# Kernel optimization log

Hardware: AMD Instinct MI355X
Metric: run time of the kernel (lower is better)

## Reference

```python
import jax, jax.numpy as jnp
import numpy as np

B, T, C, HEADS = 4, 2305, 384, 6
BN_EPS = 1e-5


def setup_inputs() -> dict:
    key = jax.random.key(0)
    ks = jax.random.split(key, 24)
    d = {
        'x': jax.random.normal(ks[0], (B, T, C), dtype=jnp.float32),
        'h': 48,
        'w': 48,
        # depthwise conv kernels (groups=C, no bias): OIHW with I=1
        'kq': jax.random.normal(ks[1], (C, 1, 3, 3), dtype=jnp.float32) * 0.1,
        'kk': jax.random.normal(ks[2], (C, 1, 3, 3), dtype=jnp.float32) * 0.1,
        'kv': jax.random.normal(ks[3], (C, 1, 3, 3), dtype=jnp.float32) * 0.1,
        # BatchNorm (eval mode) params per projection: gamma, beta, running_mean, running_var
        'gq': jax.random.normal(ks[4], (C,), dtype=jnp.float32) * 0.1 + 1.0,
        'bq': jax.random.normal(ks[5], (C,), dtype=jnp.float32) * 0.1,
        'mq': jax.random.normal(ks[6], (C,), dtype=jnp.float32) * 0.1,
        'vq': jax.random.uniform(ks[7], (C,), dtype=jnp.float32) + 0.5,
        'gk': jax.random.normal(ks[8], (C,), dtype=jnp.float32) * 0.1 + 1.0,
        'bk': jax.random.normal(ks[9], (C,), dtype=jnp.float32) * 0.1,
        'mk': jax.random.normal(ks[10], (C,), dtype=jnp.float32) * 0.1,
        'vk': jax.random.uniform(ks[11], (C,), dtype=jnp.float32) + 0.5,
        'gv': jax.random.normal(ks[12], (C,), dtype=jnp.float32) * 0.1 + 1.0,
        'bv': jax.random.normal(ks[13], (C,), dtype=jnp.float32) * 0.1,
        'mv': jax.random.normal(ks[14], (C,), dtype=jnp.float32) * 0.1,
        'vv': jax.random.uniform(ks[15], (C,), dtype=jnp.float32) + 0.5,
        # Linear weights, torch convention [out, in]; qkv_bias=False
        'Wq': jax.random.normal(ks[16], (C, C), dtype=jnp.float32) / np.sqrt(C),
        'Wk': jax.random.normal(ks[17], (C, C), dtype=jnp.float32) / np.sqrt(C),
        'Wv': jax.random.normal(ks[18], (C, C), dtype=jnp.float32) / np.sqrt(C),
        'Wo': jax.random.normal(ks[19], (C, C), dtype=jnp.float32) / np.sqrt(C),
        'bo': jax.random.normal(ks[20], (C,), dtype=jnp.float32) * 0.01,
    }
    return d


def _dw_bn(xi, kern, gamma, beta, mean, var, h, w):
    # xi: [B, C, h, w]; depthwise 3x3 conv, stride 1, pad 1, then eval-mode BN
    y = jax.lax.conv_general_dilated(
        xi, kern, window_strides=(1, 1), padding=((1, 1), (1, 1)),
        feature_group_count=C, dimension_numbers=('NCHW', 'OIHW', 'NCHW'))
    scale = (gamma / jnp.sqrt(var + BN_EPS))[None, :, None, None]
    y = (y - mean[None, :, None, None]) * scale + beta[None, :, None, None]
    # b c h w -> b (h w) c
    return y.transpose(0, 2, 3, 1).reshape(y.shape[0], h * w, C)


def _forward(x, kq, kk, kv, gq, bq, mq, vq, gk, bk, mk, vk, gv, bv, mv, vv,
             Wq, Wk, Wv, Wo, bo, h, w):
    b, t, c = x.shape
    scale = c ** (-0.5)  # note: dim**-0.5, NOT head_dim**-0.5 (as in source)
    cls_tok, xs = x[:, :1], x[:, 1:]
    xi = xs.reshape(b, h, w, c).transpose(0, 3, 1, 2)  # b (h w) c -> b c h w
    q = jnp.concatenate([cls_tok, _dw_bn(xi, kq, gq, bq, mq, vq, h, w)], axis=1)
    k = jnp.concatenate([cls_tok, _dw_bn(xi, kk, gk, bk, mk, vk, h, w)], axis=1)
    v = jnp.concatenate([cls_tok, _dw_bn(xi, kv, gv, bv, mv, vv, h, w)], axis=1)
    dh = c // HEADS
    q = (q @ Wq.T).reshape(b, t, HEADS, dh).transpose(0, 2, 1, 3)  # bhtd
    k = (k @ Wk.T).reshape(b, t, HEADS, dh).transpose(0, 2, 1, 3)
    v = (v @ Wv.T).reshape(b, t, HEADS, dh).transpose(0, 2, 1, 3)
    attn = jax.nn.softmax(jnp.einsum('bhld,bhtd->bhlt', q, k) * scale, axis=-1)
    out = jnp.einsum('bhlt,bhtd->bhld', attn, v)
    out = out.transpose(0, 2, 1, 3).reshape(b, t, c)
    return out @ Wo.T + bo


def reference(x, kq, kk, kv, gq, bq, mq, vq, gk, bk, mk, vk, gv, bv, mv, vv,
              Wq, Wk, Wv, Wo, bo, h, w):
    return _forward(x, kq, kk, kv, gq, bq, mq, vq, gk, bk, mk, vk, gv, bv,
                    mv, vv, Wq, Wk, Wv, Wo, bo, h, w)
```

## Files before the change

kernel.cpp:

```cpp
#include <hip/hip_runtime.h>
#include <hip/hip_bf16.h>

#define BN 4
#define TT 2305
#define CC 384
#define HH 6
#define DH 64
#define GW 48
#define BH (BN*HH)
#define TP 2368
#define TQP 2560
#define MF 9220
#define MP 9344
#define MB2 73
#define NSPL 2
#define C2 0.07362223f

typedef __hip_bfloat16 bf16;
typedef __attribute__((ext_vector_type(8))) short short8;
typedef __attribute__((ext_vector_type(4))) float floatx4;
typedef __attribute__((ext_vector_type(16))) float floatx16;

#define MFMA16(a,b,c) __builtin_amdgcn_mfma_f32_16x16x32_bf16((a),(b),(c),0,0,0)
#define MFMA32(a,b,c) __builtin_amdgcn_mfma_f32_32x32x16_bf16((a),(b),(c),0,0,0)

__device__ __forceinline__ unsigned pack2(float a, float b) {
    bf16 lo = __float2bfloat16(a);
    bf16 hi = __float2bfloat16(b);
    unsigned short ul = *reinterpret_cast<unsigned short*>(&lo);
    unsigned short uh = *reinterpret_cast<unsigned short*>(&hi);
    return (unsigned)ul | ((unsigned)uh << 16);
}
__device__ __forceinline__ float bu2f(unsigned u16) {
    unsigned v = u16 << 16;
    return *reinterpret_cast<float*>(&v);
}

__global__ __launch_bounds__(384)
void conv_bn(const float* __restrict__ x,
             const float* __restrict__ kq, const float* __restrict__ kk, const float* __restrict__ kv,
             const float* __restrict__ gq, const float* __restrict__ bq, const float* __restrict__ mq, const float* __restrict__ vq,
             const float* __restrict__ gk, const float* __restrict__ bk, const float* __restrict__ mk, const float* __restrict__ vk,
             const float* __restrict__ gv, const float* __restrict__ bv, const float* __restrict__ mv, const float* __restrict__ vv,
             const float* __restrict__ Wq, const float* __restrict__ Wk,
             const float* __restrict__ Wv, const float* __restrict__ Wo,
             bf16* __restrict__ wqb, bf16* __restrict__ wkb,
             bf16* __restrict__ wvb, bf16* __restrict__ wob,
             bf16* __restrict__ cq, bf16* __restrict__ ck, bf16* __restrict__ cv)
{
    {
        const int i = blockIdx.x * 384 + threadIdx.x;
        if (i < CC * CC) {
            wqb[i] = __float2bfloat16(Wq[i]);
            wkb[i] = __float2bfloat16(Wk[i]);
            wvb[i] = __float2bfloat16(Wv[i]);
            wob[i] = __float2bfloat16(Wo[i]);
        }
    }

    const int n = blockIdx.x;
    const int b = n / 289;
    const int t0 = (n % 289) * 8;
    const int c = threadIdx.x;
    const size_t xbase = (size_t)b * TT * CC;

    const float sq = gq[c] * rsqrtf(vq[c] + 1e-5f), oq = bq[c] - mq[c] * sq;
    const float sk = gk[c] * rsqrtf(vk[c] + 1e-5f), ok = bk[c] - mk[c] * sk;
    const float sv = gv[c] * rsqrtf(vv[c] + 1e-5f), ov = bv[c] - mv[c] * sv;
    float wq9[9], wk9[9], wv9[9];
    #pragma unroll
    for (int u = 0; u < 9; u++) {
        wq9[u] = kq[c * 9 + u]; wk9[u] = kk[c * 9 + u]; wv9[u] = kv[c * 9 + u];
    }

    for (int g = 0; g < 8; g++) {
        const int t = t0 + g;
        if (t >= TT) break;
        const size_t mrow = (size_t)(b * TT + t) * CC + c;
        if (t == 0) {
            bf16 xv = __float2bfloat16(x[xbase + c]);
            cq[mrow] = xv; ck[mrow] = xv; cv[mrow] = xv;
        } else {
            const int s = t - 1, i = s / GW, j = s % GW;
            float aq = 0.f, ak = 0.f, av = 0.f;
            #pragma unroll
            for (int di = 0; di < 3; di++) {
                int ii = i + di - 1;
                if (ii < 0 || ii >= GW) continue;
                #pragma unroll
                for (int dj = 0; dj < 3; dj++) {
                    int jj = j + dj - 1;
                    if (jj < 0 || jj >= GW) continue;
                    float xv = x[xbase + (size_t)(1 + ii * GW + jj) * CC + c];
                    int u = di * 3 + dj;
                    aq += xv * wq9[u]; ak += xv * wk9[u]; av += xv * wv9[u];
                }
            }
            cq[mrow] = __float2bfloat16(aq * sq + oq);
            ck[mrow] = __float2bfloat16(ak * sk + ok);
            cv[mrow] = __float2bfloat16(av * sv + ov);
        }
    }
}

__global__ __launch_bounds__(256)
void qkv_gemm(const bf16* __restrict__ cq, const bf16* __restrict__ ck, const bf16* __restrict__ cv,
              const bf16* __restrict__ Wq, const bf16* __restrict__ Wk, const bf16* __restrict__ Wv,
              bf16* __restrict__ q, bf16* __restrict__ k, bf16* __restrict__ vT)
{
    const int bt = blockIdx.x;
    const int b = bt / 10;
    const int m0 = (bt % 10) * 256;
    const int n0 = blockIdx.y * 64;
    const int w = threadIdx.x >> 6, lane = threadIdx.x & 63;
    const int lm = lane & 15, q4 = lane >> 4;
    const int which = n0 / CC;
    const int obase = n0 % CC;
    const bf16* A = (which == 0) ? cq : (which == 1) ? ck : cv;
    const bf16* W = (which == 0) ? Wq : (which == 1) ? Wk : Wv;

    __shared__ __align__(16) bf16 TR[64 * 264];

    size_t arow[4];
    #pragma unroll
    for (int st = 0; st < 4; st++) {
        int t = m0 + st * 64 + w * 16 + lm;
        if (t >= TT) t = TT - 1;
        arow[st] = (size_t)(b * TT + t) * CC;
    }

    floatx4 acc[4][4];
    #pragma unroll
    for (int st = 0; st < 4; st++)
        #pragma unroll
        for (int n = 0; n < 4; n++) acc[st][n] = (floatx4){0.f, 0.f, 0.f, 0.f};

    #pragma unroll 2
    for (int kc = 0; kc < CC / 32; kc++) {
        short8 a[4];
        #pragma unroll
        for (int st = 0; st < 4; st++)
            a[st] = *(const short8*)(A + arow[st] + kc * 32 + q4 * 8);
        #pragma unroll
        for (int n = 0; n < 4; n++) {
            short8 bfr = *(const short8*)(W + (size_t)(obase + n * 16 + lm) * CC + kc * 32 + q4 * 8);
            #pragma unroll
            for (int st = 0; st < 4; st++)
                acc[st][n] = MFMA16(a[st], bfr, acc[st][n]);
        }
    }

    if (which == 2) {
        #pragma unroll
        for (int st = 0; st < 4; st++)
            #pragma unroll
            for (int n = 0; n < 4; n++) {
                const int ol = n * 16 + lm;
                const int ml = st * 64 + w * 16 + q4 * 4;
                uint2 pkd = { pack2(acc[st][n][0], acc[st][n][1]),
                              pack2(acc[st][n][2], acc[st][n][3]) };
                *(uint2*)&TR[ol * 264 + ml] = pkd;
            }
        __syncthreads();
        const int h = obase >> 6;
        const int o = threadIdx.x >> 2;
        const int seg = threadIdx.x & 3;
        const size_t vrow = ((size_t)(b * HH + h) * DH + o) * TP;
        #pragma unroll
        for (int j = 0; j < 8; j++) {
            const int ml = seg * 64 + j * 8;
            const int t = m0 + ml;
            uint4 val = *(const uint4*)&TR[o * 264 + ml];
            if (t + 8 <= TT) {
                *(uint4*)(vT + vrow + t) = val;
            } else if (t < TT) {
                const bf16* pv = (const bf16*)&val;
                for (int e = 0; e < 8 && t + e < TT; e++) vT[vrow + t + e] = pv[e];
            }
        }
    } else {
        #pragma unroll
        for (int st = 0; st < 4; st++)
            #pragma unroll
            for (int n = 0; n < 4; n++) {
                const int o = obase + n * 16 + lm;
                const int h = o >> 6, d = o & 63;
                #pragma unroll
                for (int r = 0; r < 4; r++) {
                    const int t = m0 + st * 64 + w * 16 + q4 * 4 + r;
                    if (t >= TT) continue;
                    bf16 val = __float2bfloat16(acc[st][n][r]);
                    if (which == 0)
                        q[((size_t)(b * HH + h) * TQP + t) * DH + d] = val;
                    else
                        k[((size_t)(b * HH + h) * TP + t) * DH + d] = val;
                }
            }
    }
}

__global__ __launch_bounds__(256, 2)
void flash(const bf16* __restrict__ q, const bf16* __restrict__ k,
           const bf16* __restrict__ vT, bf16* __restrict__ OP, float* __restrict__ ML)
{
    const int id = blockIdx.x;
    const int bh = id % BH;
    const int rest = id / BH;
    const int z = rest % NSPL;
    const int qt = rest / NSPL;
    const int tid = threadIdx.x;
    const int w = tid >> 6, lane = tid & 63;
    const int q31 = lane & 31, hh = lane >> 5;
    const int q0 = qt * 256 + w * 64;
    const size_t kbase = (size_t)bh * TP * DH;
    const size_t qbase = (size_t)bh * TQP * DH;

    short8 qf[2][4];
    #pragma unroll
    for (int s = 0; s < 2; s++) {
        const bf16* qrow = q + qbase + (size_t)(q0 + s * 32 + q31) * DH;
        #pragma unroll
        for (int kc = 0; kc < 4; kc++)
            qf[s][kc] = *(const short8*)(qrow + kc * 16 + hh * 8);
    }

    floatx16 of[2][2];
    #pragma unroll
    for (int s = 0; s < 2; s++)
        #pragma unroll
        for (int dt = 0; dt < 2; dt++)
            #pragma unroll
            for (int r = 0; r < 16; r++) of[s][dt][r] = 0.f;
    float m2[2] = {-1e30f, -1e30f}, lsum[2] = {0.f, 0.f};

    const int tstart = z ? 19 : 0;
    const int tend   = z ? 37 : 19;

    for (int tc = tstart; tc < tend; tc++) {
        const int t0 = tc * 64;
        const bf16* kt = k + kbase + (size_t)t0 * DH;
        const bf16* vt = vT + kbase + t0;

        short8 ka[2][4], va[2][4];
        #pragma unroll
        for (int mt = 0; mt < 2; mt++)
            #pragma unroll
            for (int kc = 0; kc < 4; kc++) {
                const int row = mt * 32 + q31, c = 2 * kc + hh;
                ka[mt][kc] = *(const short8*)(kt + (size_t)row * DH + c * 8);
                va[mt][kc] = *(const short8*)(vt + (size_t)row * TP + c * 8);
            }
        const bool tail = (t0 + 64 > TT);

        #pragma unroll
        for (int s = 0; s < 2; s++) {
            floatx16 sv[2];
            #pragma unroll
            for (int mt = 0; mt < 2; mt++)
                #pragma unroll
                for (int r = 0; r < 16; r++) sv[mt][r] = 0.f;
            #pragma unroll
            for (int kc = 0; kc < 4; kc++) {
                sv[0] = MFMA32(ka[0][kc], qf[s][kc], sv[0]);
                sv[1] = MFMA32(ka[1][kc], qf[s][kc], sv[1]);
            }
            if (tail) {
                #pragma unroll
                for (int mt = 0; mt < 2; mt++)
                    #pragma unroll
                    for (int r = 0; r < 16; r++) {
                        const int tl = t0 + mt * 32 + (r & 3) + 8 * (r >> 2) + 4 * hh;
                        if (tl >= TT) sv[mt][r] = -1e30f;
                    }
            }
            float rm = sv[0][0];
            #pragma unroll
            for (int r = 1; r < 16; r++) rm = fmaxf(rm, sv[0][r]);
            #pragma unroll
            for (int r = 0; r < 16; r++) rm = fmaxf(rm, sv[1][r]);
            rm = fmaxf(rm, __shfl_xor(rm, 32));
            const float mn = fmaxf(m2[s], rm * C2);
            const float alpha = __builtin_amdgcn_exp2f(m2[s] - mn);
            m2[s] = mn;
            const float negm = -mn;
            float rs = 0.f;
            unsigned pk[2][8];
            #pragma unroll
            for (int mt = 0; mt < 2; mt++)
                #pragma unroll
                for (int p = 0; p < 8; p++) {
                    const float p0 = __builtin_amdgcn_exp2f(fmaf(sv[mt][2 * p], C2, negm));
                    const float p1 = __builtin_amdgcn_exp2f(fmaf(sv[mt][2 * p + 1], C2, negm));
                    rs += p0 + p1;
                    pk[mt][p] = pack2(p0, p1);
                }
            rs += __shfl_xor(rs, 32);
            lsum[s] = lsum[s] * alpha + rs;
            #pragma unroll
            for (int dt = 0; dt < 2; dt++)
                #pragma unroll
                for (int r = 0; r < 16; r++) of[s][dt][r] *= alpha;

            #pragma unroll
            for (int kc = 0; kc < 4; kc++) {
                const int u0 = 2 * kc, u1 = 2 * kc + 1;
                const unsigned P0a = pk[u0 >> 2][2 * (u0 & 3)];
                const unsigned P0b = pk[u0 >> 2][2 * (u0 & 3) + 1];
                const unsigned P1a = pk[u1 >> 2][2 * (u1 & 3)];
                const unsigned P1b = pk[u1 >> 2][2 * (u1 & 3) + 1];
                const unsigned X1 = hh ? P0a : P1a;
                const unsigned X2 = hh ? P0b : P1b;
                const unsigned Y1 = __shfl_xor(X1, 32);
                const unsigned Y2 = __shfl_xor(X2, 32);
                unsigned dw[4];
                dw[0] = hh ? Y1 : P0a;
                dw[1] = hh ? Y2 : P0b;
                dw[2] = hh ? P1a : Y1;
                dw[3] = hh ? P1b : Y2;
                short8 pb = *reinterpret_cast<short8*>(dw);
                of[s][0] = MFMA32(va[0][kc], pb, of[s][0]);
                of[s][1] = MFMA32(va[1][kc], pb, of[s][1]);
            }
        }
    }

    #pragma unroll
    for (int s = 0; s < 2; s++) {
        const int qrow = q0 + s * 32 + q31;
        if (qrow >= TT) continue;
        bf16* orow = OP + ((size_t)(z * BH + bh) * TT + qrow) * DH;
        #pragma unroll
        for (int dt = 0; dt < 2; dt++)
            #pragma unroll
            for (int p = 0; p < 4; p++) {
                const int d = dt * 32 + 8 * p + 4 * hh;
                unsigned lo = pack2(of[s][dt][4 * p], of[s][dt][4 * p + 1]);
                unsigned hi = pack2(of[s][dt][4 * p + 2], of[s][dt][4 * p + 3]);
                uint2 st = {lo, hi};
                *(uint2*)(orow + d) = st;
            }
        if (hh == 0) {
            float2 ml = {m2[s], lsum[s]};
            *(float2*)&ML[((size_t)(z * BH + bh) * TT + qrow) * 2] = ml;
        }
    }
}

__global__ __launch_bounds__(256)
void merge(const bf16* __restrict__ OP, const float* __restrict__ ML,
           bf16* __restrict__ att)
{
    const int idx = blockIdx.x * 256 + threadIdx.x;
    if (idx >= BH * TT * 16) return;
    const int quad = idx & 15;
    const int pair = idx >> 4;
    const int bh = pair / TT, row = pair % TT;
    const int b = bh / HH, h = bh % HH;
    const int d0 = quad * 4;

    float2 ml[NSPL];
    #pragma unroll
    for (int z = 0; z < NSPL; z++)
        ml[z] = *(const float2*)&ML[((size_t)(z * BH + bh) * TT + row) * 2];
    float M = ml[0].x;
    #pragma unroll
    for (int z = 1; z < NSPL; z++) M = fmaxf(M, ml[z].x);
    float wz[NSPL], den = 0.f;
    #pragma unroll
    for (int z = 0; z < NSPL; z++) {
        wz[z] = __builtin_amdgcn_exp2f(ml[z].x - M);
        den += ml[z].y * wz[z];
    }
    const float inv = 1.f / den;

    float o0 = 0.f, o1 = 0.f, o2 = 0.f, o3 = 0.f;
    #pragma unroll
    for (int z = 0; z < NSPL; z++) {
        const float s = wz[z] * inv;
        const uint2 a = *(const uint2*)&OP[((size_t)(z * BH + bh) * TT + row) * DH + d0];
        o0 += bu2f(a.x & 0xffffu) * s;
        o1 += bu2f(a.x >> 16)     * s;
        o2 += bu2f(a.y & 0xffffu) * s;
        o3 += bu2f(a.y >> 16)     * s;
    }
    uint2 st = {pack2(o0, o1), pack2(o2, o3)};
    *(uint2*)&att[((size_t)(b * TT + row) * CC) + h * DH + d0] = st;
}

__global__ __launch_bounds__(256)
void out_gemm(const bf16* __restrict__ att, const bf16* __restrict__ Wo_bf,
              const float* __restrict__ bo, float* __restrict__ out)
{
    const int m0 = blockIdx.x * 128;
    const int n0 = blockIdx.y * 64;
    const int w = threadIdx.x >> 6, lane = threadIdx.x & 63;
    const int lm = lane & 15, q4 = lane >> 4;

    const size_t ar0 = (size_t)(m0 + w * 16 + lm) * CC;
    floatx4 acc[2][4];
    #pragma unroll
    for (int st = 0; st < 2; st++)
        #pragma unroll
        for (int n = 0; n < 4; n++) acc[st][n] = (floatx4){0.f, 0.f, 0.f, 0.f};

    #pragma unroll 4
    for (int kc = 0; kc < CC / 32; kc++) {
        short8 a0 = *(const short8*)(att + ar0 + kc * 32 + q4 * 8);
        short8 a1 = *(const short8*)(att + ar0 + (size_t)64 * CC + kc * 32 + q4 * 8);
        #pragma unroll
        for (int n = 0; n < 4; n++) {
            short8 bfr = *(const short8*)(Wo_bf + (size_t)(n0 + n * 16 + lm) * CC + kc * 32 + q4 * 8);
            acc[0][n] = MFMA16(a0, bfr, acc[0][n]);
            acc[1][n] = MFMA16(a1, bfr, acc[1][n]);
        }
    }

    #pragma unroll
    for (int st = 0; st < 2; st++)
        #pragma unroll
        for (int n = 0; n < 4; n++) {
            const int o = n0 + n * 16 + lm;
            const float bias = bo[o];
            #pragma unroll
            for (int r = 0; r < 4; r++) {
                const int m = m0 + st * 64 + w * 16 + q4 * 4 + r;
                if (m < MF) out[(size_t)m * CC + o] = acc[st][n][r] + bias;
            }
        }
}

extern "C" void kernel_launch(void* const* d_in, const int* in_sizes, int n_in,
                              void* d_out, int out_size, void* d_ws, size_t ws_size,
                              hipStream_t stream)
{
    const float* x  = (const float*)d_in[0];
    const float* kq = (const float*)d_in[3];
    const float* kk = (const float*)d_in[4];
    const float* kv = (const float*)d_in[5];
    const float* gq = (const float*)d_in[6];
    const float* bq = (const float*)d_in[7];
    const float* mq = (const float*)d_in[8];
    const float* vq = (const float*)d_in[9];
    const float* gk = (const float*)d_in[10];
    const float* bk = (const float*)d_in[11];
    const float* mk = (const float*)d_in[12];
    const float* vk = (const float*)d_in[13];
    const float* gv = (const float*)d_in[14];
    const float* bv = (const float*)d_in[15];
    const float* mv = (const float*)d_in[16];
    const float* vv = (const float*)d_in[17];
    const float* Wq = (const float*)d_in[18];
    const float* Wk = (const float*)d_in[19];
    const float* Wv = (const float*)d_in[20];
    const float* Wo = (const float*)d_in[21];
    const float* bo = (const float*)d_in[22];

    char* ws = (char*)d_ws;
    const size_t SZ_CONV = (size_t)MP * CC * 2;
    const size_t SZ_Q    = (size_t)BH * TQP * DH * 2;
    const size_t SZ_K    = (size_t)BH * TP * DH * 2;
    const size_t SZ_W    = (size_t)CC * CC * 2;
    size_t off = 0;
    bf16* cq   = (bf16*)(ws + off); off += SZ_CONV;
    bf16* ck   = (bf16*)(ws + off); off += SZ_CONV;
    bf16* cv   = (bf16*)(ws + off); off += SZ_CONV;
    bf16* qb   = (bf16*)(ws + off); off += SZ_Q;
    bf16* kb   = (bf16*)(ws + off); off += SZ_K;
    bf16* vTb  = (bf16*)(ws + off); off += SZ_K;
    bf16* attb = (bf16*)(ws + off); off += SZ_CONV;
    bf16* wqb  = (bf16*)(ws + off); off += SZ_W;
    bf16* wkb  = (bf16*)(ws + off); off += SZ_W;
    bf16* wvb  = (bf16*)(ws + off); off += SZ_W;
    bf16* wob  = (bf16*)(ws + off); off += SZ_W;
    bf16*  OP = (bf16*)ws;
    float* ML = (float*)(ws + off); off += (size_t)NSPL * BH * TT * 2 * 4;

    conv_bn<<<BN * 289, 384, 0, stream>>>(x, kq, kk, kv,
                                          gq, bq, mq, vq,
                                          gk, bk, mk, vk,
                                          gv, bv, mv, vv,
                                          Wq, Wk, Wv, Wo,
                                          wqb, wkb, wvb, wob,
                                          cq, ck, cv);
    qkv_gemm<<<dim3(40, 18), 256, 0, stream>>>(cq, ck, cv, wqb, wkb, wvb, qb, kb, vTb);
    flash<<<10 * NSPL * BH, 256, 0, stream>>>(qb, kb, vTb, OP, ML);
    merge<<<(BH * TT * 16 + 255) / 256, 256, 0, stream>>>(OP, ML, attb);
    out_gemm<<<dim3(MB2, 6), 256, 0, stream>>>(attb, wob, bo, (float*)d_out);
}
```

Before: 281.9 us.

## Shrink flash query tile, split keys three ways, add lazy softmax rescale

The flash kernel now gives each wave 32 query rows instead of 64 and splits the key range into three chunks instead of two. Together with a higher occupancy hint, this raises the block count so more of the GPU is busy and fewer registers are needed per thread. It also skips the running-max rescale of the output accumulator unless some row's max grows by more than 8 in the log2 domain, and it loads V only after the QK MFMAs have been issued. The trade-offs are that each K/V tile is reused by fewer query rows, the merge step has more partial results to combine, and the Q buffer padding (TQP) shrinks. The lazy rescale lets stored probabilities exceed 1 by up to 2^8 before renormalising.

```diff
diff --git a/kernel.cpp b/kernel.cpp
--- a/kernel.cpp
+++ b/kernel.cpp
@@ -9,11 +9,12 @@
 #define GW 48
 #define BH (BN*HH)
 #define TP 2368
-#define TQP 2560
+#define TQP 2432
 #define MF 9220
 #define MP 9344
 #define MB2 73
-#define NSPL 2
+#define NSPL 3
+#define QTI 19
 #define C2 0.07362223f
 
 typedef __hip_bfloat16 bf16;
@@ -199,7 +200,7 @@
     }
 }
 
-__global__ __launch_bounds__(256, 2)
+__global__ __launch_bounds__(256, 4)
 void flash(const bf16* __restrict__ q, const bf16* __restrict__ k,
            const bf16* __restrict__ vT, bf16* __restrict__ OP, float* __restrict__ ML)
 {
@@ -211,136 +212,139 @@
     const int tid = threadIdx.x;
     const int w = tid >> 6, lane = tid & 63;
     const int q31 = lane & 31, hh = lane >> 5;
-    const int q0 = qt * 256 + w * 64;
+    const int q0 = qt * 128 + w * 32;
     const size_t kbase = (size_t)bh * TP * DH;
     const size_t qbase = (size_t)bh * TQP * DH;
 
-    short8 qf[2][4];
-    #pragma unroll
-    for (int s = 0; s < 2; s++) {
-        const bf16* qrow = q + qbase + (size_t)(q0 + s * 32 + q31) * DH;
+    short8 qf[4];
+    {
+        const bf16* qrow = q + qbase + (size_t)(q0 + q31) * DH;
         #pragma unroll
         for (int kc = 0; kc < 4; kc++)
-            qf[s][kc] = *(const short8*)(qrow + kc * 16 + hh * 8);
-    }
-
-    floatx16 of[2][2];
-    #pragma unroll
-    for (int s = 0; s < 2; s++)
-        #pragma unroll
-        for (int dt = 0; dt < 2; dt++)
-            #pragma unroll
-            for (int r = 0; r < 16; r++) of[s][dt][r] = 0.f;
-    float m2[2] = {-1e30f, -1e30f}, lsum[2] = {0.f, 0.f};
-
-    const int tstart = z ? 19 : 0;
-    const int tend   = z ? 37 : 19;
+            qf[kc] = *(const short8*)(qrow + kc * 16 + hh * 8);
+    }
+
+    floatx16 of[2];
+    #pragma unroll
+    for (int dt = 0; dt < 2; dt++)
+        #pragma unroll
+        for (int r = 0; r < 16; r++) of[dt][r] = 0.f;
+    float m2 = -1e30f, lsum = 0.f;
+
+    const int tstart = (z == 0) ? 0 : 13 + (z - 1) * 12;
+    const int tend   = (z == 0) ? 13 : 13 + z * 12;
 
     for (int tc = tstart; tc < tend; tc++) {
         const int t0 = tc * 64;
         const bf16* kt = k + kbase + (size_t)t0 * DH;
         const bf16* vt = vT + kbase + t0;
 
-        short8 ka[2][4], va[2][4];
+        short8 ka[2][4];
         #pragma unroll
         for (int mt = 0; mt < 2; mt++)
             #pragma unroll
-            for (int kc = 0; kc < 4; kc++) {
-                const int row = mt * 32 + q31, c = 2 * kc + hh;
-                ka[mt][kc] = *(const short8*)(kt + (size_t)row * DH + c * 8);
-                va[mt][kc] = *(const short8*)(vt + (size_t)row * TP + c * 8);
-            }
-        const bool tail = (t0 + 64 > TT);
-
-        #pragma unroll
-        for (int s = 0; s < 2; s++) {
-            floatx16 sv[2];
+            for (int kc = 0; kc < 4; kc++)
+                ka[mt][kc] = *(const short8*)(kt + (size_t)(mt * 32 + q31) * DH + (2 * kc + hh) * 8);
+
+        floatx16 sv[2];
+        #pragma unroll
+        for (int mt = 0; mt < 2; mt++)
+            #pragma unroll
+            for (int r = 0; r < 16; r++) sv[mt][r] = 0.f;
+        #pragma unroll
+        for (int kc = 0; kc < 4; kc++) {
+            sv[0] = MFMA32(ka[0][kc], qf[kc], sv[0]);
+            sv[1] = MFMA32(ka[1][kc], qf[kc], sv[1]);
+        }
+
+        short8 va[2][4];
+        #pragma unroll
+        for (int mt = 0; mt < 2; mt++)
+            #pragma unroll
+            for (int kc = 0; kc < 4; kc++)
+                va[mt][kc] = *(const short8*)(vt + (size_t)(mt * 32 + q31) * TP + (2 * kc + hh) * 8);
+
+        if (t0 + 64 > TT) {
             #pragma unroll
             for (int mt = 0; mt < 2; mt++)
                 #pragma unroll
-                for (int r = 0; r < 16; r++) sv[mt][r] = 0.f;
-            #pragma unroll
-            for (int kc = 0; kc < 4; kc++) {
-                sv[0] = MFMA32(ka[0][kc], qf[s][kc], sv[0]);
-                sv[1] = MFMA32(ka[1][kc], qf[s][kc], sv[1]);
-            }
-            if (tail) {
-                #pragma unroll
-                for (int mt = 0; mt < 2; mt++)
-                    #pragma unroll
-                    for (int r = 0; r < 16; r++) {
-                        const int tl = t0 + mt * 32 + (r & 3) + 8 * (r >> 2) + 4 * hh;
-                        if (tl >= TT) sv[mt][r] = -1e30f;
-                    }
-            }
-            float rm = sv[0][0];
-            #pragma unroll
-            for (int r = 1; r < 16; r++) rm = fmaxf(rm, sv[0][r]);
-            #pragma unroll
-            for (int r = 0; r < 16; r++) rm = fmaxf(rm, sv[1][r]);
-            rm = fmaxf(rm, __shfl_xor(rm, 32));
-            const float mn = fmaxf(m2[s], rm * C2);
-            const float alpha = __builtin_amdgcn_exp2f(m2[s] - mn);
-            m2[s] = mn;
-            const float negm = -mn;
-            float rs = 0.f;
-            unsigned pk[2][8];
-            #pragma unroll
-            for (int mt = 0; mt < 2; mt++)
-                #pragma unroll
-                for (int p = 0; p < 8; p++) {
-                    const float p0 = __builtin_amdgcn_exp2f(fmaf(sv[mt][2 * p], C2, negm));
-                    const float p1 = __builtin_amdgcn_exp2f(fmaf(sv[mt][2 * p + 1], C2, negm));
-                    rs += p0 + p1;
-                    pk[mt][p] = pack2(p0, p1);
+                for (int r = 0; r < 16; r++) {
+                    const int tl = t0 + mt * 32 + (r & 3) + 8 * (r >> 2) + 4 * hh;
+                    if (tl >= TT) sv[mt][r] = -1e30f;
                 }
-            rs += __shfl_xor(rs, 32);
-            lsum[s] = lsum[s] * alpha + rs;
+        }
+
+        float rm = sv[0][0];
+        #pragma unroll
+        for (int r = 1; r < 16; r++) rm = fmaxf(rm, sv[0][r]);
+        #pragma unroll
+        for (int r = 0; r < 16; r++) rm = fmaxf(rm, sv[1][r]);
+        rm = fmaxf(rm, __shfl_xor(rm, 32));
+        const float rms = rm * C2;
+
+        if (!__all(rms <= m2 + 8.f)) {
+            const float mn = fmaxf(m2, rms);
+            const float alpha = __builtin_amdgcn_exp2f(m2 - mn);
+            m2 = mn;
+            lsum *= alpha;
             #pragma unroll
             for (int dt = 0; dt < 2; dt++)
                 #pragma unroll
-                for (int r = 0; r < 16; r++) of[s][dt][r] *= alpha;
-
-            #pragma unroll
-            for (int kc = 0; kc < 4; kc++) {
-                const int u0 = 2 * kc, u1 = 2 * kc + 1;
-                const unsigned P0a = pk[u0 >> 2][2 * (u0 & 3)];
-                const unsigned P0b = pk[u0 >> 2][2 * (u0 & 3) + 1];
-                const unsigned P1a = pk[u1 >> 2][2 * (u1 & 3)];
-                const unsigned P1b = pk[u1 >> 2][2 * (u1 & 3) + 1];
-                const unsigned X1 = hh ? P0a : P1a;
-                const unsigned X2 = hh ? P0b : P1b;
-                const unsigned Y1 = __shfl_xor(X1, 32);
-                const unsigned Y2 = __shfl_xor(X2, 32);
-                unsigned dw[4];
-                dw[0] = hh ? Y1 : P0a;
-                dw[1] = hh ? Y2 : P0b;
-                dw[2] = hh ? P1a : Y1;
-                dw[3] = hh ? P1b : Y2;
-                short8 pb = *reinterpret_cast<short8*>(dw);
-                of[s][0] = MFMA32(va[0][kc], pb, of[s][0]);
-                of[s][1] = MFMA32(va[1][kc], pb, of[s][1]);
-            }
-        }
-    }
-
-    #pragma unroll
-    for (int s = 0; s < 2; s++) {
-        const int qrow = q0 + s * 32 + q31;
-        if (qrow >= TT) continue;
+                for (int r = 0; r < 16; r++) of[dt][r] *= alpha;
+        }
+        const float negm = -m2;
+
+        float rs = 0.f;
+        unsigned pk[2][8];
+        #pragma unroll
+        for (int mt = 0; mt < 2; mt++)
+            #pragma unroll
+            for (int p = 0; p < 8; p++) {
+                const float p0 = __builtin_amdgcn_exp2f(fmaf(sv[mt][2 * p], C2, negm));
+                const float p1 = __builtin_amdgcn_exp2f(fmaf(sv[mt][2 * p + 1], C2, negm));
+                rs += p0 + p1;
+                pk[mt][p] = pack2(p0, p1);
+            }
+        rs += __shfl_xor(rs, 32);
+        lsum += rs;
+
+        #pragma unroll
+        for (int kc = 0; kc < 4; kc++) {
+            const int u0 = 2 * kc, u1 = 2 * kc + 1;
+            const unsigned P0a = pk[u0 >> 2][2 * (u0 & 3)];
+            const unsigned P0b = pk[u0 >> 2][2 * (u0 & 3) + 1];
+            const unsigned P1a = pk[u1 >> 2][2 * (u1 & 3)];
+            const unsigned P1b = pk[u1 >> 2][2 * (u1 & 3) + 1];
+            const unsigned X1 = hh ? P0a : P1a;
+            const unsigned X2 = hh ? P0b : P1b;
+            const unsigned Y1 = __shfl_xor(X1, 32);
+            const unsigned Y2 = __shfl_xor(X2, 32);
+            unsigned dw[4];
+            dw[0] = hh ? Y1 : P0a;
+            dw[1] = hh ? Y2 : P0b;
+            dw[2] = hh ? P1a : Y1;
+            dw[3] = hh ? P1b : Y2;
+            short8 pb = *reinterpret_cast<short8*>(dw);
+            of[0] = MFMA32(va[0][kc], pb, of[0]);
+            of[1] = MFMA32(va[1][kc], pb, of[1]);
+        }
+    }
+
+    const int qrow = q0 + q31;
+    if (qrow < TT) {
         bf16* orow = OP + ((size_t)(z * BH + bh) * TT + qrow) * DH;
         #pragma unroll
         for (int dt = 0; dt < 2; dt++)
             #pragma unroll
             for (int p = 0; p < 4; p++) {
                 const int d = dt * 32 + 8 * p + 4 * hh;
-                unsigned lo = pack2(of[s][dt][4 * p], of[s][dt][4 * p + 1]);
-                unsigned hi = pack2(of[s][dt][4 * p + 2], of[s][dt][4 * p + 3]);
+                unsigned lo = pack2(of[dt][4 * p], of[dt][4 * p + 1]);
+                unsigned hi = pack2(of[dt][4 * p + 2], of[dt][4 * p + 3]);
                 uint2 st = {lo, hi};
                 *(uint2*)(orow + d) = st;
             }
         if (hh == 0) {
-            float2 ml = {m2[s], lsum[s]};
+            float2 ml = {m2, lsum};
             *(float2*)&ML[((size_t)(z * BH + bh) * TT + qrow) * 2] = ml;
         }
     }
@@ -483,7 +487,7 @@
                                           wqb, wkb, wvb, wob,
                                           cq, ck, cv);
     qkv_gemm<<<dim3(40, 18), 256, 0, stream>>>(cq, ck, cv, wqb, wkb, wvb, qb, kb, vTb);
-    flash<<<10 * NSPL * BH, 256, 0, stream>>>(qb, kb, vTb, OP, ML);
+    flash<<<QTI * NSPL * BH, 256, 0, stream>>>(qb, kb, vTb, OP, ML);
     merge<<<(BH * TT * 16 + 255) / 256, 256, 0, stream>>>(OP, ML, attb);
     out_gemm<<<dim3(MB2, 6), 256, 0, stream>>>(attb, wob, bo, (float*)d_out);
 }
```

Measured after the change: 355.7 us. 26.2% more time.
